# Kernel tuning notes

Measured on AMD Instinct MI355X. Metric: run time of the kernel, lower is better.

## Reference

```python
import jax, jax.numpy as jnp
import numpy as np

N = 200000
IN_CH = 128
HIDDEN = [512, 512, 256]
NUM_TYPES = 10


def hetero_linear(x, types, W, b):
    # y[n] = x[n] @ W[types[n]] + b[types[n]]
    # Loop over the small fixed set of types (grouped GEMM as masked dense GEMMs).
    out = jnp.zeros((x.shape[0], W.shape[2]), dtype=x.dtype)
    for t in range(W.shape[0]):
        yt = x @ W[t] + b[t]
        out = out + jnp.where((types == t)[:, None], yt, jnp.zeros((), x.dtype))
    return out


def setup_inputs() -> dict:
    key = jax.random.key(0)
    ks = jax.random.split(key, 8)
    dims = [IN_CH] + HIDDEN
    inp = {
        "x": jax.random.normal(ks[0], (N, IN_CH), dtype=jnp.float32),
        "atom_types": jax.random.randint(ks[1], (N,), 0, NUM_TYPES, dtype=jnp.int32),
    }
    for i in range(3):
        fan_in = dims[i]
        scale = 1.0 / np.sqrt(fan_in)
        inp[f"W{i}"] = jax.random.normal(ks[2 + 2 * i], (NUM_TYPES, dims[i], dims[i + 1]), dtype=jnp.float32) * scale
        inp[f"b{i}"] = jax.random.normal(ks[3 + 2 * i], (NUM_TYPES, dims[i + 1]), dtype=jnp.float32) * scale
    return inp


def reference(x, atom_types, W0, b0, W1, b1, W2, b2):
    h = jax.nn.relu(hetero_linear(x, atom_types, W0, b0))
    h = jax.nn.relu(hetero_linear(h, atom_types, W1, b1))
    return hetero_linear(h, atom_types, W2, b2)
```

## Files before the change

kernel.cpp:

```cpp
#include <hip/hip_runtime.h>
#include <stdint.h>

typedef float  f32x4  __attribute__((ext_vector_type(4)));
typedef short  bf16x8 __attribute__((ext_vector_type(8)));

#define TYPES 10
#define D_IN  128
#define D_H1  512
#define D_H2  512
#define D_OUT 256

__device__ __forceinline__ unsigned short f2bf(float f) {
  union { float f; unsigned u; } v; v.f = f;
  unsigned u = v.u;
  return (unsigned short)((u + 0x7FFFu + ((u >> 16) & 1u)) >> 16);
}

__device__ __forceinline__ void async16(void* lds, const void* g) {
  __builtin_amdgcn_global_load_lds(
      (const __attribute__((address_space(1))) void*)g,
      (__attribute__((address_space(3))) void*)lds, 16, 0, 0);
}

__global__ void k_init(int* meta) {
  if (threadIdx.x < 48) meta[threadIdx.x] = 0;
}

__global__ void k_hist(const int* __restrict__ types, int n, int* __restrict__ meta) {
  __shared__ int lc[TYPES];
  if (threadIdx.x < TYPES) lc[threadIdx.x] = 0;
  __syncthreads();
  int i = blockIdx.x * 256 + threadIdx.x;
  if (i < n) atomicAdd(&lc[types[i]], 1);
  __syncthreads();
  if (threadIdx.x < TYPES && lc[threadIdx.x]) atomicAdd(&meta[threadIdx.x], lc[threadIdx.x]);
}

__global__ void k_scan(int* meta) {
  if (threadIdx.x == 0) {
    int off = 0;
    for (int t = 0; t < TYPES; ++t) {
      meta[16 + t] = off;
      off += ((meta[t] + 255) >> 8) << 8;
    }
    meta[26] = off;
  }
}

__global__ void k_scatter(const int* __restrict__ types, int n,
                          int* __restrict__ meta, int* __restrict__ perm) {
  __shared__ int lc[TYPES], lbase[TYPES];
  if (threadIdx.x < TYPES) lc[threadIdx.x] = 0;
  __syncthreads();
  int i = blockIdx.x * 256 + threadIdx.x;
  int t = 0, loc = 0;
  bool ok = i < n;
  if (ok) { t = types[i]; loc = atomicAdd(&lc[t], 1); }
  __syncthreads();
  if (threadIdx.x < TYPES) {
    int c = lc[threadIdx.x];
    lbase[threadIdx.x] = c ? atomicAdd(&meta[32 + threadIdx.x], c) : 0;
  }
  __syncthreads();
  if (ok) perm[meta[16 + t] + lbase[t] + loc] = i;
}

__global__ void k_wtrans_all(const float* __restrict__ W0a, const float* __restrict__ W1a,
                             const float* __restrict__ W2a,
                             unsigned short* __restrict__ wt0, unsigned short* __restrict__ wt1,
                             unsigned short* __restrict__ wt2) {
  int b = blockIdx.x;
  const float* W; unsigned short* Wt; int K, NOUT, t, local;
  if (b < 160)      { W = W0a; Wt = wt0; K = 128; NOUT = 512; t = b / 16; local = b % 16; }
  else if (b < 800) { b -= 160; W = W1a; Wt = wt1; K = 512; NOUT = 512; t = b / 64; local = b % 64; }
  else              { b -= 800; W = W2a; Wt = wt2; K = 512; NOUT = 256; t = b / 32; local = b % 32; }
  int ntn = NOUT >> 6;
  int kb = local / ntn, nb = local % ntn;
  __shared__ unsigned short tile[64][65];
  const float* src = W + (size_t)t * K * NOUT + (size_t)(kb * 64) * NOUT + nb * 64;
  int c = threadIdx.x & 63;
  int r0 = threadIdx.x >> 6;
  #pragma unroll
  for (int i = 0; i < 16; ++i) {
    int r = r0 * 16 + i;
    tile[r][c] = f2bf(src[(size_t)r * NOUT + c]);
  }
  __syncthreads();
  unsigned short* dst = Wt + (size_t)t * NOUT * K + (size_t)(nb * 64) * K + kb * 64;
  #pragma unroll
  for (int i = 0; i < 16; ++i) {
    int nn = r0 * 16 + i;
    dst[(size_t)nn * K + c] = tile[c][nn];
  }
}

__launch_bounds__(512, 2)
__global__ void k_gemm1(const float* __restrict__ x,
                        const unsigned short* __restrict__ Wt,
                        const float* __restrict__ bias,
                        unsigned short* __restrict__ H,
                        const int* __restrict__ meta,
                        const int* __restrict__ perm) {
  constexpr int K = 128, NOUT = 512;
  __shared__ char lds[131072];

  int NXB = gridDim.x;
  int nwg = NXB * (int)gridDim.y;
  int raw = blockIdx.x + blockIdx.y * NXB;
  int q = nwg >> 3, rr = nwg & 7;
  int xcd = raw & 7, idx = raw >> 3;
  int swz = (xcd < rr ? xcd * (q + 1) : rr * (q + 1) + (xcd - rr) * q) + idx;
  int bx = swz % NXB, by = swz / NXB;

  int row0 = by * 256;
  if (row0 >= meta[26]) return;
  int t = 0;
  while (row0 >= meta[17 + t]) t++;
  int seg = meta[16 + t], cnt = meta[t];
  int tid = threadIdx.x, lane = tid & 63, wid = tid >> 6;
  int wr = (wid >> 2) * 128, wc = (wid & 3) * 64;
  int ah = wid >> 2, bh = (wid & 3) >> 1;
  int col0 = bx * 256;
  const char* Bg = (const char*)(Wt + ((size_t)t * NOUT + col0) * K);

  int gl = tid & 7, lrb = tid >> 3;
  int gsrc = (gl ^ (lrb & 7)) * 16;
  const char* bS = Bg + (size_t)lrb * (2 * K) + gsrc;

  #pragma unroll
  for (int h = 0; h < 2; ++h)
    #pragma unroll
    for (int kt = 0; kt < 2; ++kt) {
      char* dst = lds + 65536 + (h * 2 + kt) * 16384 + wid * 1024;
      const char* src = bS + (size_t)(h * 128) * (2 * K) + kt * 128;
      async16(dst,        src);
      async16(dst + 8192, src + (size_t)64 * (2 * K));
    }

  #pragma unroll
  for (int h = 0; h < 2; ++h)
    #pragma unroll
    for (int i = 0; i < 2; ++i) {
      int lr = i * 64 + lrb;
      int p = row0 + h * 128 + lr;
      bool ok = (unsigned)(p - seg) < (unsigned)cnt;
      int sr = ok ? perm[p] : 0;
      int ksw = (gl ^ (lr & 7)) * 8;
      #pragma unroll
      for (int kt = 0; kt < 2; ++kt) {
        bf16x8 v;
        if (ok) {
          const float* sp = x + (size_t)sr * K + kt * 64 + ksw;
          float4 f0 = *(const float4*)(sp);
          float4 f1 = *(const float4*)(sp + 4);
          v[0] = (short)f2bf(f0.x); v[1] = (short)f2bf(f0.y);
          v[2] = (short)f2bf(f0.z); v[3] = (short)f2bf(f0.w);
          v[4] = (short)f2bf(f1.x); v[5] = (short)f2bf(f1.y);
          v[6] = (short)f2bf(f1.z); v[7] = (short)f2bf(f1.w);
        } else {
          v = bf16x8{0, 0, 0, 0, 0, 0, 0, 0};
        }
        *(bf16x8*)(lds + (h * 2 + kt) * 16384 + lr * 128 + gl * 16) = v;
      }
    }

  __syncthreads();

  f32x4 acc[8][4] = {};
  int rA = lane & 15, qoff = (lane >> 4) * 16, xr = (lane & 7) << 4;
  #pragma unroll
  for (int kt = 0; kt < 2; ++kt) {
    const char* Au = lds + (ah * 2 + kt) * 16384;
    const char* Bu = lds + 65536 + (bh * 2 + kt) * 16384;
    bf16x8 b0[4], b1[4];
    #pragma unroll
    for (int n = 0; n < 4; ++n) {
      int cl = (wid & 1) * 64 + n * 16 + rA;
      b0[n] = *(const bf16x8*)(Bu + cl * 128 + (qoff ^ xr));
      b1[n] = *(const bf16x8*)(Bu + cl * 128 + ((64 + qoff) ^ xr));
    }
    #pragma unroll
    for (int mh = 0; mh < 2; ++mh) {
      bf16x8 a0[4], a1[4];
      #pragma unroll
      for (int m = 0; m < 4; ++m) {
        int lr = mh * 64 + m * 16 + rA;
        a0[m] = *(const bf16x8*)(Au + lr * 128 + (qoff ^ xr));
        a1[m] = *(const bf16x8*)(Au + lr * 128 + ((64 + qoff) ^ xr));
      }
      #pragma unroll
      for (int m = 0; m < 4; ++m)
        #pragma unroll
        for (int n = 0; n < 4; ++n) {
          acc[mh * 4 + m][n] = __builtin_amdgcn_mfma_f32_16x16x32_bf16(a0[m], b0[n], acc[mh * 4 + m][n], 0, 0, 0);
          acc[mh * 4 + m][n] = __builtin_amdgcn_mfma_f32_16x16x32_bf16(a1[m], b1[n], acc[mh * 4 + m][n], 0, 0, 0);
        }
    }
  }
  __builtin_amdgcn_s_barrier();

  int cA = lane & 15, rE = (lane >> 4) * 4;
  float bv[4];
  #pragma unroll
  for (int ni = 0; ni < 4; ++ni) bv[ni] = bias[t * NOUT + col0 + wc + ni * 16 + cA];
  char* cb = (char*)lds;
  #pragma unroll
  for (int mi = 0; mi < 8; ++mi) {
    int rowoff = (mi >> 2) * 64 + (mi & 3) * 16;
    #pragma unroll
    for (int e = 0; e < 4; ++e) {
      int row = wr + rowoff + rE + e;
      int sw = (row & 7) << 4;
      #pragma unroll
      for (int ni = 0; ni < 4; ++ni) {
        float v = fmaxf(acc[mi][ni][e] + bv[ni], 0.f);
        int col = wc + ni * 16 + cA;
        *(unsigned short*)(cb + ((row * 512 + col * 2) ^ sw)) = f2bf(v);
      }
    }
  }
  __builtin_amdgcn_s_barrier();
  #pragma unroll 4
  for (int r = 0; r < 16; ++r) {
    int row = wid * 32 + r * 2 + (lane >> 5);
    int addr = row * 512 + ((((lane & 31) * 16)) ^ ((row & 7) << 4));
    bf16x8 v = *(const bf16x8*)(cb + addr);
    *(bf16x8*)(H + (size_t)(row0 + row) * NOUT + col0 + (lane & 31) * 8) = v;
  }
}

template <int K, int NOUT, bool RELU, bool FINAL>
__launch_bounds__(512, 2)
__global__ void k_gemm(const unsigned short* __restrict__ A,
                       const unsigned short* __restrict__ Wt,
                       const float* __restrict__ bias,
                       unsigned short* __restrict__ H,
                       float* __restrict__ OUT,
                       const int* __restrict__ meta,
                       const int* __restrict__ perm) {
  constexpr int nKT = K / 64;
  __shared__ char lds[131072];

  int NXB = gridDim.x;
  int nwg = NXB * (int)gridDim.y;
  int raw = blockIdx.x + blockIdx.y * NXB;
  int q = nwg >> 3, rr = nwg & 7;
  int xcd = raw & 7, idx = raw >> 3;
  int swz = (xcd < rr ? xcd * (q + 1) : rr * (q + 1) + (xcd - rr) * q) + idx;
  int bx = swz % NXB, by = swz / NXB;

  int row0 = by * 256;
  if (row0 >= meta[26]) return;
  int t = 0;
  while (row0 >= meta[17 + t]) t++;
  int seg = meta[16 + t], cnt = meta[t];
  int tid = threadIdx.x, lane = tid & 63, wid = tid >> 6;
  int wr = (wid >> 2) * 128, wc = (wid & 3) * 64;
  int ah = wid >> 2, bh = (wid & 3) >> 1, clb = (wid & 1) * 64;
  int col0 = bx * 256;
  const char* Ag = (const char*)(A + (size_t)row0 * K);
  const char* Bg = (const char*)(Wt + ((size_t)t * NOUT + col0) * K);

  int gsrc = ((tid & 7) ^ ((tid >> 3) & 7)) * 16;
  const char* aS = Ag + (size_t)(tid >> 3) * (2 * K) + gsrc;
  const char* bS = Bg + (size_t)(tid >> 3) * (2 * K) + gsrc;

  auto stage = [&](int kt, int sub) {
    if (kt >= nKT) return;
    int h = sub & 1, du = kt & 1;
    char* dst = lds + ((sub < 2) ? 0 : 65536) + (du * 2 + h) * 16384 + wid * 1024;
    const char* base = (sub < 2) ? aS : bS;
    const char* src = base + (size_t)(h * 128) * (2 * K) + (size_t)kt * 128;
    async16(dst,        src);
    async16(dst + 8192, src + (size_t)64 * (2 * K));
  };

  f32x4 acc[8][4] = {};
  int rA = lane & 15, qoff = (lane >> 4) * 16, xr = (lane & 7) << 4;

  stage(0, 0); stage(0, 1); stage(0, 2); stage(0, 3); stage(1, 0);
  asm volatile("s_waitcnt vmcnt(2)" ::: "memory");
  __builtin_amdgcn_s_barrier();

  for (int g = 0; g < nKT; ++g) {
    int d = g & 1;
    const char* Au = lds + (d * 2 + ah) * 16384;
    const char* Bu = lds + 65536 + (d * 2 + bh) * 16384;
    bf16x8 a[4], b0[4], b1[4];

    #pragma unroll
    for (int m = 0; m < 4; ++m) {
      int lr = m * 16 + rA;
      a[m] = *(const bf16x8*)(Au + lr * 128 + (qoff ^ xr));
    }
    #pragma unroll
    for (int n = 0; n < 4; ++n) {
      int cl = clb + n * 16 + rA;
      b0[n] = *(const bf16x8*)(Bu + cl * 128 + (qoff ^ xr));
      b1[n] = *(const bf16x8*)(Bu + cl * 128 + ((64 + qoff) ^ xr));
    }
    stage(g + 1, 1);
    asm volatile("s_waitcnt lgkmcnt(8)" ::: "memory");
    __builtin_amdgcn_s_barrier();
    asm volatile("s_waitcnt lgkmcnt(0)" ::: "memory");
    __builtin_amdgcn_s_setprio(1);
    #pragma unroll
    for (int m = 0; m < 4; ++m)
      #pragma unroll
      for (int n = 0; n < 4; ++n)
        acc[m][n] = __builtin_amdgcn_mfma_f32_16x16x32_bf16(a[m], b0[n], acc[m][n], 0, 0, 0);
    __builtin_amdgcn_s_setprio(0);
    __builtin_amdgcn_s_barrier();

    #pragma unroll
    for (int m = 0; m < 4; ++m) {
      int lr = m * 16 + rA;
      a[m] = *(const bf16x8*)(Au + lr * 128 + ((64 + qoff) ^ xr));
    }
    stage(g + 1, 2);
    __builtin_amdgcn_s_barrier();
    asm volatile("s_waitcnt lgkmcnt(0)" ::: "memory");
    __builtin_amdgcn_s_setprio(1);
    #pragma unroll
    for (int m = 0; m < 4; ++m)
      #pragma unroll
      for (int n = 0; n < 4; ++n)
        acc[m][n] = __builtin_amdgcn_mfma_f32_16x16x32_bf16(a[m], b1[n], acc[m][n], 0, 0, 0);
    __builtin_amdgcn_s_setprio(0);
    __builtin_amdgcn_s_barrier();

    #pragma unroll
    for (int m = 0; m < 4; ++m) {
      int lr = 64 + m * 16 + rA;
      a[m] = *(const bf16x8*)(Au + lr * 128 + (qoff ^ xr));
    }
    stage(g + 1, 3);
    __builtin_amdgcn_s_barrier();
    asm volatile("s_waitcnt lgkmcnt(0)" ::: "memory");
    __builtin_amdgcn_s_setprio(1);
    #pragma unroll
    for (int m = 0; m < 4; ++m)
      #pragma unroll
      for (int n = 0; n < 4; ++n)
        acc[4 + m][n] = __builtin_amdgcn_mfma_f32_16x16x32_bf16(a[m], b0[n], acc[4 + m][n], 0, 0, 0);
    __builtin_amdgcn_s_setprio(0);
    __builtin_amdgcn_s_barrier();

    #pragma unroll
    for (int m = 0; m < 4; ++m) {
      int lr = 64 + m * 16 + rA;
      a[m] = *(const bf16x8*)(Au + lr * 128 + ((64 + qoff) ^ xr));
    }
    stage(g + 2, 0);
    __builtin_amdgcn_s_barrier();
    asm volatile("s_waitcnt lgkmcnt(0)" ::: "memory");
    __builtin_amdgcn_s_setprio(1);
    #pragma unroll
    for (int m = 0; m < 4; ++m)
      #pragma unroll
      for (int n = 0; n < 4; ++n)
        acc[4 + m][n] = __builtin_amdgcn_mfma_f32_16x16x32_bf16(a[m], b1[n], acc[4 + m][n], 0, 0, 0);
    __builtin_amdgcn_s_setprio(0);
    if (g + 1 < nKT) {
      if (g + 2 < nKT) asm volatile("s_waitcnt vmcnt(2)" ::: "memory");
      else             asm volatile("s_waitcnt vmcnt(0)" ::: "memory");
    }
    __builtin_amdgcn_s_barrier();
  }

  int cA = lane & 15, rE = (lane >> 4) * 4;
  float bv[4];
  #pragma unroll
  for (int ni = 0; ni < 4; ++ni) bv[ni] = bias[t * NOUT + col0 + wc + ni * 16 + cA];
  char* cb = (char*)lds;

  if (!FINAL) {
    #pragma unroll
    for (int mi = 0; mi < 8; ++mi) {
      int rowoff = (mi >> 2) * 64 + (mi & 3) * 16;
      #pragma unroll
      for (int e = 0; e < 4; ++e) {
        int row = wr + rowoff + rE + e;
        int sw = (row & 7) << 4;
        #pragma unroll
        for (int ni = 0; ni < 4; ++ni) {
          float v = acc[mi][ni][e] + bv[ni];
          if (RELU) v = fmaxf(v, 0.f);
          int col = wc + ni * 16 + cA;
          *(unsigned short*)(cb + ((row * 512 + col * 2) ^ sw)) = f2bf(v);
        }
      }
    }
    __builtin_amdgcn_s_barrier();
    #pragma unroll 4
    for (int r = 0; r < 16; ++r) {
      int row = wid * 32 + r * 2 + (lane >> 5);
      int addr = row * 512 + ((((lane & 31) * 16)) ^ ((row & 7) << 4));
      bf16x8 v = *(const bf16x8*)(cb + addr);
      *(bf16x8*)(H + (size_t)(row0 + row) * NOUT + col0 + (lane & 31) * 8) = v;
    }
  } else {
    int myhalf = (wid & 3) >> 1;
    #pragma unroll
    for (int p = 0; p < 2; ++p) {
      if (myhalf == p) {
        int colh = wc & 127;
        #pragma unroll
        for (int mi = 0; mi < 8; ++mi) {
          int rowoff = (mi >> 2) * 64 + (mi & 3) * 16;
          #pragma unroll
          for (int e = 0; e < 4; ++e) {
            int row = wr + rowoff + rE + e;
            int sw = (row & 7) << 4;
            #pragma unroll
            for (int ni = 0; ni < 4; ++ni) {
              float v = acc[mi][ni][e] + bv[ni];
              if (RELU) v = fmaxf(v, 0.f);
              int col = colh + ni * 16 + cA;
              *(float*)(cb + ((row * 512 + col * 4) ^ sw)) = v;
            }
          }
        }
      }
      __builtin_amdgcn_s_barrier();
      #pragma unroll 4
      for (int r = 0; r < 16; ++r) {
        int row = wid * 32 + r * 2 + (lane >> 5);
        int gr = row0 + row;
        int addr = row * 512 + ((((lane & 31) * 16)) ^ ((row & 7) << 4));
        float4 v = *(const float4*)(cb + addr);
        if (gr - seg < cnt) {
          int pr = perm[gr];
          *(float4*)(OUT + (size_t)pr * NOUT + p * (NOUT / 2) + (lane & 31) * 4) = v;
        }
      }
      if (p == 0) __builtin_amdgcn_s_barrier();
    }
  }
}

extern "C" void kernel_launch(void* const* d_in, const int* in_sizes, int n_in,
                              void* d_out, int out_size, void* d_ws, size_t ws_size,
                              hipStream_t stream) {
  const float* x     = (const float*)d_in[0];
  const int*   types = (const int*)d_in[1];
  const float* W0    = (const float*)d_in[2];
  const float* b0    = (const float*)d_in[3];
  const float* W1    = (const float*)d_in[4];
  const float* b1    = (const float*)d_in[5];
  const float* W2    = (const float*)d_in[6];
  const float* b2    = (const float*)d_in[7];
  float* out = (float*)d_out;
  int n = in_sizes[1];
  int RB = (n + 255) / 256 + TYPES;
  size_t NPAD = (size_t)RB * 256;

  char* ws = (char*)d_ws;
  int* meta = (int*)ws;
  int* perm = (int*)(ws + 1024);
  size_t off = 1024 + NPAD * 4;
  off = (off + 255) & ~(size_t)255;
  unsigned short* wt0 = (unsigned short*)(ws + off); off += (size_t)TYPES * D_H1 * D_IN * 2;
  unsigned short* wt1 = (unsigned short*)(ws + off); off += (size_t)TYPES * D_H2 * D_H1 * 2;
  unsigned short* wt2 = (unsigned short*)(ws + off); off += (size_t)TYPES * D_OUT * D_H2 * 2;
  off = (off + 255) & ~(size_t)255;
  unsigned short* B1 = (unsigned short*)(ws + off); off += NPAD * 512 * 2;
  unsigned short* B2 = (unsigned short*)(ws + off); off += NPAD * 512 * 2;

  int hb = (n + 255) / 256;
  k_init<<<1, 64, 0, stream>>>(meta);
  k_hist<<<hb, 256, 0, stream>>>(types, n, meta);
  k_scan<<<1, 64, 0, stream>>>(meta);
  k_scatter<<<hb, 256, 0, stream>>>(types, n, meta, perm);
  k_wtrans_all<<<1120, 256, 0, stream>>>(W0, W1, W2, wt0, wt1, wt2);

  k_gemm1<<<dim3(D_H1 / 256, RB), 512, 0, stream>>>(x, wt0, b0, B2, meta, perm);
  k_gemm<D_H1, D_H2, true,  false><<<dim3(D_H2 / 256, RB), 512, 0, stream>>>(B2, wt1, b1, B1, nullptr, meta, perm);
  k_gemm<D_H2, D_OUT, false, true ><<<dim3(D_OUT / 256, RB), 512, 0, stream>>>(B1, wt2, b2, nullptr, out, meta, perm);
}
```

Baseline: 428.5 us.

## Add occupancy-oriented 256x128 tile GEMM for middle hidden layer

Replaces the templated GEMM for the second layer (512->512) with a dedicated kernel that uses 256x128 output tiles, a 48KB double-buffered LDS footprint and launch bounds allowing four workgroups per CU. The grid doubles along the column dimension. The aim is more resident waves to hide memory latency, traded against re-reading each A tile for twice as many column blocks and a smaller K-step per barrier. The epilogue stages results through LDS in two row halves to fit the reduced buffer.

```diff
diff --git a/kernel.cpp b/kernel.cpp
--- a/kernel.cpp
+++ b/kernel.cpp
@@ -226,6 +226,121 @@
     int addr = row * 512 + ((((lane & 31) * 16)) ^ ((row & 7) << 4));
     bf16x8 v = *(const bf16x8*)(cb + addr);
     *(bf16x8*)(H + (size_t)(row0 + row) * NOUT + col0 + (lane & 31) * 8) = v;
+  }
+}
+
+__launch_bounds__(512, 4)
+__global__ void k_gemmO(const unsigned short* __restrict__ A,
+                        const unsigned short* __restrict__ Wt,
+                        const float* __restrict__ bias,
+                        unsigned short* __restrict__ H,
+                        const int* __restrict__ meta) {
+  constexpr int K = 512, NOUT = 512, nKT = 16;
+  __shared__ char lds[49152];
+
+  int NXB = gridDim.x;
+  int nwg = NXB * (int)gridDim.y;
+  int raw = blockIdx.x + blockIdx.y * NXB;
+  int q = nwg >> 3, rr = nwg & 7;
+  int xcd = raw & 7, idx = raw >> 3;
+  int swz = (xcd < rr ? xcd * (q + 1) : rr * (q + 1) + (xcd - rr) * q) + idx;
+  int bx = swz % NXB, by = swz / NXB;
+
+  int row0 = by * 256;
+  if (row0 >= meta[26]) return;
+  int t = 0;
+  while (row0 >= meta[17 + t]) t++;
+  int tid = threadIdx.x, lane = tid & 63, wid = tid >> 6;
+  int wrow = (wid >> 1) * 64, wcol = (wid & 1) * 64;
+  int col0 = bx * 128;
+  const char* Ag = (const char*)(A + (size_t)row0 * K);
+  const char* Bg = (const char*)(Wt + ((size_t)t * NOUT + col0) * K);
+
+  int gswz = ((tid & 3) ^ ((tid >> 3) & 3)) * 16;
+  const char* aS = Ag + (size_t)(tid >> 2) * (2 * K) + gswz;
+  const char* bS = Bg + (size_t)(tid >> 2) * (2 * K) + gswz;
+
+  auto stage = [&](int kt) {
+    if (kt >= nKT) return;
+    int d = kt & 1;
+    #pragma unroll
+    for (int i = 0; i < 2; ++i)
+      async16(lds + d * 16384 + i * 8192 + wid * 1024,
+              aS + (size_t)(i * 128) * (2 * K) + kt * 64);
+    async16(lds + 32768 + d * 8192 + wid * 1024, bS + kt * 64);
+  };
+
+  f32x4 acc[4][4] = {};
+  int rA = lane & 15, qk = lane >> 4;
+  int rsw = ((rA >> 1) & 3);
+
+  stage(0);
+  asm volatile("s_waitcnt vmcnt(0)" ::: "memory");
+  __builtin_amdgcn_s_barrier();
+
+  for (int g = 0; g < nKT; ++g) {
+    int d = g & 1;
+    const char* Ad = lds + d * 16384;
+    const char* Bd = lds + 32768 + d * 8192;
+    __builtin_amdgcn_sched_barrier(0);
+    bf16x8 a[4], b[4];
+    #pragma unroll
+    for (int m = 0; m < 4; ++m) {
+      int row = wrow + m * 16 + rA;
+      a[m] = *(const bf16x8*)(Ad + row * 64 + ((qk ^ rsw) * 16));
+    }
+    #pragma unroll
+    for (int n = 0; n < 4; ++n) {
+      int col = wcol + n * 16 + rA;
+      b[n] = *(const bf16x8*)(Bd + col * 64 + ((qk ^ rsw) * 16));
+    }
+    stage(g + 1);
+    __builtin_amdgcn_s_barrier();
+    asm volatile("s_waitcnt lgkmcnt(0)" ::: "memory");
+    __builtin_amdgcn_sched_barrier(0);
+    __builtin_amdgcn_s_setprio(1);
+    #pragma unroll
+    for (int m = 0; m < 4; ++m)
+      #pragma unroll
+      for (int n = 0; n < 4; ++n)
+        acc[m][n] = __builtin_amdgcn_mfma_f32_16x16x32_bf16(a[m], b[n], acc[m][n], 0, 0, 0);
+    __builtin_amdgcn_s_setprio(0);
+    asm volatile("s_waitcnt vmcnt(0)" ::: "memory");
+    __builtin_amdgcn_s_barrier();
+  }
+
+  int cA = lane & 15, rE = (lane >> 4) * 4;
+  float bv[4];
+  #pragma unroll
+  for (int ni = 0; ni < 4; ++ni) bv[ni] = bias[t * NOUT + col0 + wcol + ni * 16 + cA];
+  char* cb = (char*)lds;
+  #pragma unroll
+  for (int rh = 0; rh < 2; ++rh) {
+    if ((wid >> 2) == rh) {
+      #pragma unroll
+      for (int m = 0; m < 4; ++m)
+        #pragma unroll
+        for (int e = 0; e < 4; ++e) {
+          int lrow = ((wid >> 1) & 1) * 64 + m * 16 + rE + e;
+          int sw = (lrow & 7) << 4;
+          #pragma unroll
+          for (int ni = 0; ni < 4; ++ni) {
+            float v = fmaxf(acc[m][ni][e] + bv[ni], 0.f);
+            int col = wcol + ni * 16 + cA;
+            *(unsigned short*)(cb + ((lrow * 256 + col * 2) ^ sw)) = f2bf(v);
+          }
+        }
+    }
+    __builtin_amdgcn_s_barrier();
+    #pragma unroll
+    for (int k = 0; k < 4; ++k) {
+      int gidx = k * 512 + tid;
+      int lrow = gidx >> 4, gc = gidx & 15;
+      int addr = lrow * 256 + ((gc * 16) ^ ((lrow & 7) << 4));
+      bf16x8 v = *(const bf16x8*)(cb + addr);
+      *(bf16x8*)(H + (size_t)(row0 + rh * 128 + lrow) * NOUT + col0 + gc * 8) = v;
+    }
+    if (rh == 0) __builtin_amdgcn_s_barrier();
   }
 }
 
@@ -475,6 +590,6 @@
   k_wtrans_all<<<1120, 256, 0, stream>>>(W0, W1, W2, wt0, wt1, wt2);
 
   k_gemm1<<<dim3(D_H1 / 256, RB), 512, 0, stream>>>(x, wt0, b0, B2, meta, perm);
-  k_gemm<D_H1, D_H2, true,  false><<<dim3(D_H2 / 256, RB), 512, 0, stream>>>(B2, wt1, b1, B1, nullptr, meta, perm);
+  k_gemmO<<<dim3(D_H2 / 128, RB), 512, 0, stream>>>(B2, wt1, b1, B1, meta);
   k_gemm<D_H2, D_OUT, false, true ><<<dim3(D_OUT / 256, RB), 512, 0, stream>>>(B1, wt2, b2, nullptr, out, meta, perm);
 }
```

Result: slower. 439.8 us (+2.6%).
